# Performance work log

Measured on AMD Instinct MI355X. Metric: run time of the kernel, lower is better.

Reference implementation:

```python
import jax, jax.numpy as jnp
import numpy as np

VOCAB = 65
N_EMBD = 32
HEAD = 16
BLOCK = 8
B = 65536


def setup_inputs() -> dict:
    key = jax.random.key(0)
    ks = jax.random.split(key, 12)
    idx = jax.random.randint(ks[0], (B, BLOCK), 0, VOCAB)
    targets = jax.random.randint(ks[1], (B, BLOCK), 0, VOCAB)
    s = 0.02
    tok_emb = jax.random.normal(ks[2], (VOCAB, N_EMBD), jnp.float32) * s
    pos_emb = jax.random.normal(ks[3], (BLOCK, N_EMBD), jnp.float32) * s
    Wk = jax.random.normal(ks[4], (N_EMBD, HEAD), jnp.float32) * s
    bk = jnp.zeros((HEAD,), jnp.float32)
    Wq = jax.random.normal(ks[5], (N_EMBD, HEAD), jnp.float32) * s
    bq = jnp.zeros((HEAD,), jnp.float32)
    Wv = jax.random.normal(ks[6], (N_EMBD, HEAD), jnp.float32) * s
    bv = jnp.zeros((HEAD,), jnp.float32)
    Wlm = jax.random.normal(ks[7], (HEAD, VOCAB), jnp.float32) * s
    blm = jnp.zeros((VOCAB,), jnp.float32)
    return {"idx": idx, "targets": targets, "tok_emb": tok_emb, "pos_emb": pos_emb,
            "Wk": Wk, "bk": bk, "Wq": Wq, "bq": bq, "Wv": Wv, "bv": bv,
            "Wlm": Wlm, "blm": blm}


def reference(idx, targets, tok_emb, pos_emb, Wk, bk, Wq, bq, Wv, bv, Wlm, blm):
    Bsz, T = idx.shape
    x = tok_emb[idx] + pos_emb[None, :T, :]                  # (B,T,C)
    k = x @ Wk + bk                                          # (B,T,H)
    q = x @ Wq + bq
    wei = jnp.einsum('bth,bsh->bts', q, k) * (HEAD ** -0.5)  # (B,T,T)
    tril = jnp.tril(jnp.ones((T, T), bool))
    wei = jnp.where(tril[None], wei, -jnp.inf)
    # NOTE: original torch code uses F.softmax(wei, dim=1) — over the QUERY axis.
    wei = jax.nn.softmax(wei, axis=1)
    v = x @ Wv + bv
    attn = jnp.einsum('bts,bsh->bth', wei, v)                # (B,T,H)
    logits = attn @ Wlm + blm                                # (B,T,V)
    logits_flat = logits.reshape(Bsz * T, VOCAB)
    tgt_flat = targets.reshape(Bsz * T)
    logp = jax.nn.log_softmax(logits_flat, axis=-1)
    loss = -jnp.mean(jnp.take_along_axis(logp, tgt_flat[:, None], axis=-1))
    return logits_flat, loss
```

## Files before the change

### kernel.cpp

```cpp
#include <hip/hip_runtime.h>

#define NVOC 65
#define NE   32
#define HD   16
#define NB   65536
#define NROWS (NB * 8)
#define NLOG  (NROWS * NVOC)


static __device__ __forceinline__ float readlane_f(float v, int l) {
  return __uint_as_float(__builtin_amdgcn_readlane(__float_as_uint(v), l));
}

__global__ __launch_bounds__(1024) void bigram_tables(
    const float* __restrict__ tok, const float* __restrict__ pos,
    const float* __restrict__ Wk, const float* __restrict__ bk,
    const float* __restrict__ Wq, const float* __restrict__ bq,
    const float* __restrict__ Wv, const float* __restrict__ bv,
    const float* __restrict__ Wlm, float* __restrict__ ws)
{
  __shared__ float S[8416];
  const int tid = threadIdx.x;
  const int bid = blockIdx.x;
  for (int o = tid; o < 2080; o += 1024) S[o] = tok[o];
  for (int o = tid; o < 256;  o += 1024) S[2080 + o] = pos[o];
  for (int o = tid; o < 512;  o += 1024) {
    S[2336 + o] = Wq[o]; S[2848 + o] = Wk[o]; S[3360 + o] = Wv[o];
  }
  for (int o = tid; o < 1040; o += 1024) S[3872 + o] = Wlm[o];
  __syncthreads();

  for (int o = tid; o < 1168; o += 1024) {
    if (o < 1040) {
      const int a = o >> 4, h = o & 15;
      float sq = 0.f, sk = 0.f, sv = 0.f;
      #pragma unroll
      for (int c = 0; c < NE; ++c) {
        const float e = S[a*32 + c];
        sq = fmaf(e, S[2336 + c*16 + h], sq);
        sk = fmaf(e, S[2848 + c*16 + h], sk);
        sv = fmaf(e, S[3360 + c*16 + h], sv);
      }
      S[4912 + o] = sq; S[5952 + o] = sk; S[6992 + o] = sv;
    } else {
      const int o2 = o - 1040, t = o2 >> 4, h = o2 & 15;
      float sq = bq[h], sk = bk[h], sv = bv[h];
      #pragma unroll
      for (int c = 0; c < NE; ++c) {
        const float e = S[2080 + t*32 + c];
        sq = fmaf(e, S[2336 + c*16 + h], sq);
        sk = fmaf(e, S[2848 + c*16 + h], sk);
        sv = fmaf(e, S[3360 + c*16 + h], sv);
      }
      S[8032 + o2] = sq; S[8160 + o2] = sk; S[8288 + o2] = sv;
    }
  }
  __syncthreads();

  float* wsTab = ws + 16;
  const int lo = bid * 632;
  const int hi = (lo + 632 < 10074) ? lo + 632 : 10074;
  for (int o = lo + tid; o < hi; o += 1024) {
    float r = 0.f; int dst;
    if (o < 4225) {
      const int a = o / 65, b = o % 65;
      #pragma unroll
      for (int h = 0; h < HD; ++h) r = fmaf(S[4912 + a*16 + h], S[5952 + b*16 + h], r);
      r *= 0.25f; dst = o;
    } else if (o < 4745) {
      const int o2 = o - 4225, a = o2 >> 3, s2 = o2 & 7;
      #pragma unroll
      for (int h = 0; h < HD; ++h) r = fmaf(S[4912 + a*16 + h], S[8160 + s2*16 + h], r);
      r *= 0.25f; dst = 8450 + o2;
    } else if (o < 5265) {
      const int o2 = o - 4745, t2 = o2 / 65, b = o2 % 65;
      #pragma unroll
      for (int h = 0; h < HD; ++h) r = fmaf(S[8032 + t2*16 + h], S[5952 + b*16 + h], r);
      r *= 0.25f; dst = 8970 + o2;
    } else if (o < 5329) {
      const int o2 = o - 5265, t2 = o2 >> 3, s2 = o2 & 7;
      #pragma unroll
      for (int h = 0; h < HD; ++h) r = fmaf(S[8032 + t2*16 + h], S[8160 + s2*16 + h], r);
      r *= 0.25f; dst = 9490 + o2;
    } else if (o < 9554) {
      const int o2 = o - 5329, a = o2 / 65, j = o2 % 65;
      #pragma unroll
      for (int h = 0; h < HD; ++h) r = fmaf(S[6992 + a*16 + h], S[3872 + h*65 + j], r);
      dst = 4225 + o2;
    } else {
      const int o2 = o - 9554, s2 = o2 / 65, j = o2 % 65;
      #pragma unroll
      for (int h = 0; h < HD; ++h) r = fmaf(S[8288 + s2*16 + h], S[3872 + h*65 + j], r);
      dst = o;
    }
    wsTab[dst] = r;
  }
}

__global__ __launch_bounds__(512, 8) void bigram_main(
    const int* __restrict__ idx, const int* __restrict__ tgt,
    const float* __restrict__ blm, const float* __restrict__ ws,
    float* __restrict__ wsout, float* __restrict__ out)
{
  __shared__ __align__(16) float S[10074];
  __shared__ float red[8];
  const int tid = threadIdx.x;
  const int lane = tid & 63;
  const int w    = tid >> 6;
  const int t    = lane >> 3;
  const int s    = lane & 7;
  const int u    = lane & 7;
  const int gw = blockIdx.x * 8 + w;
  const int iv = idx[gw*64 + lane];
  const int tv = tgt[gw*64 + lane];
  const float blmj  = blm[lane];
  const float blm64 = blm[64];
  const float* wsTab = ws + 16;
  {
    const float4* t4 = (const float4*)wsTab;
    float4* s4 = (float4*)S;
    for (int o = tid; o < 2518; o += 512) s4[o] = t4[o];
    if (tid < 2) S[10072 + tid] = wsTab[10072 + tid];
  }
  __syncthreads();

  const int gwu = __builtin_amdgcn_readfirstlane(gw);
  float* __restrict__ outw = out + (size_t)gwu * 4160u;
  const unsigned l65p64 = (unsigned)lane * 65u + 64u;
  const bool lane8m = (lane < 8);

  const float g4 = S[9490 + lane];
  float pvl[8], pvl64[8];
  #pragma unroll
  for (int k = 0; k < 8; ++k) {
    pvl[k]   = S[9554 + k*65 + lane];
    pvl64[k] = S[9554 + k*65 + 64];
  }
  const bool b0 = (lane & 1) != 0, b1 = (lane & 2) != 0, b2 = (lane & 4) != 0;

  float wsm_cur;
  {
    const int av  = __shfl(iv, s);
    const int a_t = __shfl(iv, t);
    float wr = S[a_t*65 + av] + S[8450 + a_t*8 + s] + S[8970 + t*65 + av] + g4;
    float e = (t >= s) ? __expf(wr) : 0.f;
    float sm = e;
    sm += __shfl_xor(sm, 8); sm += __shfl_xor(sm, 16); sm += __shfl_xor(sm, 32);
    wsm_cur = __fdividef(e, sm);
  }

  float acc_lsm = 0.f, tl = 0.f;
  for (int itb = 0; itb < 8; ++itb) {
    const int base  = itb * 8;
    const int basen = ((itb + 1) & 7) * 8;
    float msr[8], Ms64[8];
    #pragma unroll
    for (int k = 0; k < 8; ++k) {
      const int ak = __builtin_amdgcn_readlane(iv, base + k);
      msr[k]  = S[4225 + ak*65 + lane];
      Ms64[k] = S[4225 + ak*65 + 64] + pvl64[k];
    }
    const int av_n  = __shfl(iv, basen + s);
    const int a_tn  = __shfl(iv, basen + t);
    float Ms[8];
    #pragma unroll
    for (int k = 0; k < 8; ++k) Ms[k] = msr[k] + pvl[k];
    const float wr_n = S[a_tn*65 + av_n] + S[8450 + a_tn*8 + s]
                     + S[8970 + t*65 + av_n] + g4;
    float e_n = (t >= s) ? __expf(wr_n) : 0.f;
    float lg64v = blm64;
    #pragma unroll
    for (int k = 0; k < 8; ++k) {
      const float wk_row = __shfl(wsm_cur, u*8 + k);
      lg64v = fmaf(wk_row, Ms64[k], lg64v);
    }
    float sm_n = e_n;
    sm_n += __shfl_xor(sm_n, 8);
    const unsigned vo = (unsigned)itb * 520u + (unsigned)lane;
    if (lane8m) outw[(unsigned)itb * 520u + l65p64] = lg64v;
    {
      const int tgu = __shfl(tv, base + u);
      tl += (lane8m && tgu == 64) ? lg64v : 0.f;
    }
    float ee[8];
    #pragma unroll
    for (int tt = 0; tt < 4; ++tt) {
      float lg = blmj;
      #pragma unroll
      for (int k = 0; k <= tt; ++k) {
        const float wk = readlane_f(wsm_cur, tt*8 + k);
        lg = fmaf(wk, Ms[k], lg);
      }
      outw[vo + tt*65] = lg;
      ee[tt] = __expf(lg);
      const int tg = __builtin_amdgcn_readlane(tv, base + tt);
      tl += (lane == tg) ? lg : 0.f;
    }
    sm_n += __shfl_xor(sm_n, 16);
    #pragma unroll
    for (int tt = 4; tt < 8; ++tt) {
      float lg = blmj;
      #pragma unroll
      for (int k = 0; k <= tt; ++k) {
        const float wk = readlane_f(wsm_cur, tt*8 + k);
        lg = fmaf(wk, Ms[k], lg);
      }
      outw[vo + tt*65] = lg;
      ee[tt] = __expf(lg);
      const int tg = __builtin_amdgcn_readlane(tv, base + tt);
      tl += (lane == tg) ? lg : 0.f;
    }
    sm_n += __shfl_xor(sm_n, 32);
    float k0 = b0 ? ee[1] : ee[0], s0 = b0 ? ee[0] : ee[1];
    float k1 = b0 ? ee[3] : ee[2], s1 = b0 ? ee[2] : ee[3];
    float k2 = b0 ? ee[5] : ee[4], s2 = b0 ? ee[4] : ee[5];
    float k3 = b0 ? ee[7] : ee[6], s3 = b0 ? ee[6] : ee[7];
    k0 += __shfl_xor(s0, 1); k1 += __shfl_xor(s1, 1);
    k2 += __shfl_xor(s2, 1); k3 += __shfl_xor(s3, 1);
    float m0 = b1 ? k1 : k0, t0 = b1 ? k0 : k1;
    float m1 = b1 ? k3 : k2, t1 = b1 ? k2 : k3;
    m0 += __shfl_xor(t0, 2); m1 += __shfl_xor(t1, 2);
    float r = b2 ? m1 : m0,  t2 = b2 ? m0 : m1;
    r += __shfl_xor(t2, 4);
    if (lane8m) r += __expf(lg64v);
    r += __shfl_xor(r, 8); r += __shfl_xor(r, 16); r += __shfl_xor(r, 32);
    acc_lsm += __log2f(r);
    wsm_cur = __fdividef(e_n, sm_n);
  }
  float v = acc_lsm * (0.6931471805599453f * 0.125f) - tl;
  v += __shfl_xor(v, 1); v += __shfl_xor(v, 2);  v += __shfl_xor(v, 4);
  v += __shfl_xor(v, 8); v += __shfl_xor(v, 16); v += __shfl_xor(v, 32);
  if (lane == 0) red[w] = v;
  __syncthreads();
  if (tid == 0) {
    wsout[10112 + blockIdx.x] = red[0] + red[1] + red[2] + red[3]
                              + red[4] + red[5] + red[6] + red[7];
  }
}

__global__ __launch_bounds__(1024) void bigram_fin2(
    const float* __restrict__ ws, float* __restrict__ out)
{
  __shared__ float r[16];
  const int tid = threadIdx.x;
  float v = ws[10112 + tid];
  v += __shfl_xor(v, 1); v += __shfl_xor(v, 2);  v += __shfl_xor(v, 4);
  v += __shfl_xor(v, 8); v += __shfl_xor(v, 16); v += __shfl_xor(v, 32);
  if ((tid & 63) == 0) r[tid >> 6] = v;
  __syncthreads();
  if (tid == 0) {
    float a = 0.f;
    #pragma unroll
    for (int i = 0; i < 16; ++i) a += r[i];
    out[NLOG] = a * (1.0f / (float)NROWS);
  }
}

extern "C" void kernel_launch(void* const* d_in, const int* in_sizes, int n_in,
                              void* d_out, int out_size, void* d_ws, size_t ws_size,
                              hipStream_t stream) {
  const int* idx = (const int*)d_in[0];
  const int* tgt = (const int*)d_in[1];
  float* ws = (float*)d_ws;
  float* out = (float*)d_out;

  bigram_tables<<<16, 1024, 0, stream>>>((const float*)d_in[2], (const float*)d_in[3],
                                         (const float*)d_in[4], (const float*)d_in[5],
                                         (const float*)d_in[6], (const float*)d_in[7],
                                         (const float*)d_in[8], (const float*)d_in[9],
                                         (const float*)d_in[10], ws);
  bigram_main<<<1024, 512, 0, stream>>>(idx, tgt, (const float*)d_in[11], ws, ws, out);
  bigram_fin2<<<1, 1024, 0, stream>>>(ws, out);
}
```

Before: 180.7 us.

## Use DPP/swizzle/permlane reductions and software-pipeline row softmax reduction

```diff
diff --git a/kernel.cpp b/kernel.cpp
--- a/kernel.cpp
+++ b/kernel.cpp
@@ -10,6 +10,29 @@
 
 static __device__ __forceinline__ float readlane_f(float v, int l) {
   return __uint_as_float(__builtin_amdgcn_readlane(__float_as_uint(v), l));
+}
+template<int C>
+static __device__ __forceinline__ float dppx(float x) {
+  return __int_as_float(__builtin_amdgcn_update_dpp(
+      __float_as_int(x), __float_as_int(x), C, 0xF, 0xF, true));
+}
+#define DPP_X1 0xB1
+#define DPP_X2 0x4E
+template<int P>
+static __device__ __forceinline__ float swz(float x) {
+  return __int_as_float(__builtin_amdgcn_ds_swizzle(__float_as_int(x), P));
+}
+#define SWZ_X4 0x101F
+#define SWZ_X8 0x201F
+static __device__ __forceinline__ float permsum16(float x) {
+  auto pr = __builtin_amdgcn_permlane16_swap(__float_as_uint(x),
+                                             __float_as_uint(x), false, false);
+  return __uint_as_float(pr[0]) + __uint_as_float(pr[1]);
+}
+static __device__ __forceinline__ float permsum32(float x) {
+  auto pr = __builtin_amdgcn_permlane32_swap(__float_as_uint(x),
+                                             __float_as_uint(x), false, false);
+  return __uint_as_float(pr[0]) + __uint_as_float(pr[1]);
 }
 
 __global__ __launch_bounds__(1024) void bigram_tables(
@@ -109,10 +132,12 @@
   const int w    = tid >> 6;
   const int t    = lane >> 3;
   const int s    = lane & 7;
-  const int u    = lane & 7;
   const int gw = blockIdx.x * 8 + w;
-  const int iv = idx[gw*64 + lane];
-  const int tv = tgt[gw*64 + lane];
+  const int gwu = __builtin_amdgcn_readfirstlane(gw);
+  const int* __restrict__ idxw = idx + (gwu << 6);
+  const int* __restrict__ tgtw = tgt + (gwu << 6);
+  const int iv = idxw[lane];
+  const int tv = tgtw[lane];
   const float blmj  = blm[lane];
   const float blm64 = blm[64];
   const float* wsTab = ws + 16;
@@ -124,109 +149,99 @@
   }
   __syncthreads();
 
-  const int gwu = __builtin_amdgcn_readfirstlane(gw);
   float* __restrict__ outw = out + (size_t)gwu * 4160u;
-  const unsigned l65p64 = (unsigned)lane * 65u + 64u;
-  const bool lane8m = (lane < 8);
+  const bool s8   = (s == 0);
+  const bool diag = (t == s);
+  const unsigned vo64 = (unsigned)t * 65u + 64u;
 
   const float g4 = S[9490 + lane];
-  float pvl[8], pvl64[8];
+  float pvl[8];
   #pragma unroll
-  for (int k = 0; k < 8; ++k) {
-    pvl[k]   = S[9554 + k*65 + lane];
-    pvl64[k] = S[9554 + k*65 + 64];
-  }
+  for (int k = 0; k < 8; ++k) pvl[k] = S[9554 + k*65 + lane];
+  const float pvl64s = S[9554 + s*65 + 64];
   const bool b0 = (lane & 1) != 0, b1 = (lane & 2) != 0, b2 = (lane & 4) != 0;
 
-  float wsm_cur;
-  {
-    const int av  = __shfl(iv, s);
-    const int a_t = __shfl(iv, t);
-    float wr = S[a_t*65 + av] + S[8450 + a_t*8 + s] + S[8970 + t*65 + av] + g4;
-    float e = (t >= s) ? __expf(wr) : 0.f;
-    float sm = e;
-    sm += __shfl_xor(sm, 8); sm += __shfl_xor(sm, 16); sm += __shfl_xor(sm, 32);
-    wsm_cur = __fdividef(e, sm);
-  }
-
   float acc_lsm = 0.f, tl = 0.f;
-  for (int itb = 0; itb < 8; ++itb) {
-    const int base  = itb * 8;
-    const int basen = ((itb + 1) & 7) * 8;
-    float msr[8], Ms64[8];
-    #pragma unroll
-    for (int k = 0; k < 8; ++k) {
-      const int ak = __builtin_amdgcn_readlane(iv, base + k);
-      msr[k]  = S[4225 + ak*65 + lane];
-      Ms64[k] = S[4225 + ak*65 + 64] + pvl64[k];
-    }
-    const int av_n  = __shfl(iv, basen + s);
-    const int a_tn  = __shfl(iv, basen + t);
-    float Ms[8];
-    #pragma unroll
-    for (int k = 0; k < 8; ++k) Ms[k] = msr[k] + pvl[k];
-    const float wr_n = S[a_tn*65 + av_n] + S[8450 + a_tn*8 + s]
-                     + S[8970 + t*65 + av_n] + g4;
-    float e_n = (t >= s) ? __expf(wr_n) : 0.f;
-    float lg64v = blm64;
-    #pragma unroll
-    for (int k = 0; k < 8; ++k) {
-      const float wk_row = __shfl(wsm_cur, u*8 + k);
-      lg64v = fmaf(wk_row, Ms64[k], lg64v);
-    }
-    float sm_n = e_n;
-    sm_n += __shfl_xor(sm_n, 8);
-    const unsigned vo = (unsigned)itb * 520u + (unsigned)lane;
-    if (lane8m) outw[(unsigned)itb * 520u + l65p64] = lg64v;
-    {
-      const int tgu = __shfl(tv, base + u);
-      tl += (lane8m && tgu == 64) ? lg64v : 0.f;
-    }
-    float ee[8];
-    #pragma unroll
-    for (int tt = 0; tt < 4; ++tt) {
-      float lg = blmj;
-      #pragma unroll
-      for (int k = 0; k <= tt; ++k) {
-        const float wk = readlane_f(wsm_cur, tt*8 + k);
-        lg = fmaf(wk, Ms[k], lg);
-      }
-      outw[vo + tt*65] = lg;
-      ee[tt] = __expf(lg);
-      const int tg = __builtin_amdgcn_readlane(tv, base + tt);
-      tl += (lane == tg) ? lg : 0.f;
-    }
-    sm_n += __shfl_xor(sm_n, 16);
-    #pragma unroll
-    for (int tt = 4; tt < 8; ++tt) {
-      float lg = blmj;
-      #pragma unroll
-      for (int k = 0; k <= tt; ++k) {
-        const float wk = readlane_f(wsm_cur, tt*8 + k);
-        lg = fmaf(wk, Ms[k], lg);
-      }
-      outw[vo + tt*65] = lg;
-      ee[tt] = __expf(lg);
-      const int tg = __builtin_amdgcn_readlane(tv, base + tt);
-      tl += (lane == tg) ? lg : 0.f;
-    }
-    sm_n += __shfl_xor(sm_n, 32);
+  float eeP[8];
+  float lg64P = 0.f;
+  auto reduce_row = [&](const float* ee, float lg64) {
     float k0 = b0 ? ee[1] : ee[0], s0 = b0 ? ee[0] : ee[1];
     float k1 = b0 ? ee[3] : ee[2], s1 = b0 ? ee[2] : ee[3];
     float k2 = b0 ? ee[5] : ee[4], s2 = b0 ? ee[4] : ee[5];
     float k3 = b0 ? ee[7] : ee[6], s3 = b0 ? ee[6] : ee[7];
-    k0 += __shfl_xor(s0, 1); k1 += __shfl_xor(s1, 1);
-    k2 += __shfl_xor(s2, 1); k3 += __shfl_xor(s3, 1);
+    k0 += dppx<DPP_X1>(s0); k1 += dppx<DPP_X1>(s1);
+    k2 += dppx<DPP_X1>(s2); k3 += dppx<DPP_X1>(s3);
     float m0 = b1 ? k1 : k0, t0 = b1 ? k0 : k1;
     float m1 = b1 ? k3 : k2, t1 = b1 ? k2 : k3;
-    m0 += __shfl_xor(t0, 2); m1 += __shfl_xor(t1, 2);
-    float r = b2 ? m1 : m0,  t2 = b2 ? m0 : m1;
-    r += __shfl_xor(t2, 4);
-    if (lane8m) r += __expf(lg64v);
-    r += __shfl_xor(r, 8); r += __shfl_xor(r, 16); r += __shfl_xor(r, 32);
+    m0 += dppx<DPP_X2>(t0); m1 += dppx<DPP_X2>(t1);
+    float r = b2 ? m1 : m0,  t2v = b2 ? m0 : m1;
+    r += swz<SWZ_X4>(t2v);
+    if (diag) r += __expf(lg64);
+    r += swz<SWZ_X8>(r);
+    r = permsum16(r); r = permsum32(r);
     acc_lsm += __log2f(r);
+  };
+
+  float wsm_cur; int av_cur;
+  {
+    const int av0 = idxw[s];
+    const int at0 = idxw[t];
+    const float wr = S[at0*65 + av0] + S[8450 + at0*8 + s]
+                   + S[8970 + t*65 + av0] + g4;
+    const float e = (t >= s) ? __expf(wr) : 0.f;
+    float sm = e + swz<SWZ_X8>(e);
+    sm = permsum16(sm); sm = permsum32(sm);
+    wsm_cur = __fdividef(e, sm);
+    av_cur = av0;
+  }
+
+  for (int itb = 0; itb < 8; ++itb) {
+    const int base  = itb * 8;
+    const int basen = ((itb + 1) & 7) * 8;
+    const int av_n = idxw[basen + s];
+    const int at_n = idxw[basen + t];
+    const int tg_c = tgtw[base + t];
+    float ms[8];
+    #pragma unroll
+    for (int k = 0; k < 8; ++k) {
+      const int ak = __builtin_amdgcn_readlane(iv, base + k);
+      ms[k] = S[4225 + ak*65 + lane];
+    }
+    const float m64 = S[4225 + av_cur*65 + 64] + pvl64s;
+    if (itb > 0) reduce_row(eeP, lg64P);
+    const float wr_n = S[at_n*65 + av_n] + S[8450 + at_n*8 + s]
+                     + S[8970 + t*65 + av_n] + g4;
+    const float e_n = (t >= s) ? __expf(wr_n) : 0.f;
+    float c64 = wsm_cur * m64;
+    c64 += dppx<DPP_X1>(c64);
+    c64 += dppx<DPP_X2>(c64);
+    c64 += swz<SWZ_X4>(c64);
+    const float lg64v = c64 + blm64;
+    if (s8) outw[(unsigned)(base*65) + vo64] = lg64v;
+    tl += (s8 && tg_c == 64) ? lg64v : 0.f;
+    float sm_n = e_n + swz<SWZ_X8>(e_n);
+    #pragma unroll
+    for (int k = 0; k < 8; ++k) ms[k] += pvl[k];
+    const unsigned vo = (unsigned)(base*65) + (unsigned)lane;
+    #pragma unroll
+    for (int tt = 0; tt < 8; ++tt) {
+      float lg = blmj;
+      #pragma unroll
+      for (int k = 0; k <= tt; ++k) {
+        const float wk = readlane_f(wsm_cur, tt*8 + k);
+        lg = fmaf(wk, ms[k], lg);
+      }
+      outw[vo + tt*65] = lg;
+      eeP[tt] = __expf(lg);
+      const int tg = __builtin_amdgcn_readlane(tv, base + tt);
+      tl += (lane == tg) ? lg : 0.f;
+    }
+    sm_n = permsum16(sm_n); sm_n = permsum32(sm_n);
     wsm_cur = __fdividef(e_n, sm_n);
-  }
+    av_cur  = av_n;
+    lg64P   = lg64v;
+  }
+  reduce_row(eeP, lg64P);
   float v = acc_lsm * (0.6931471805599453f * 0.125f) - tl;
   v += __shfl_xor(v, 1); v += __shfl_xor(v, 2);  v += __shfl_xor(v, 4);
   v += __shfl_xor(v, 8); v += __shfl_xor(v, 16); v += __shfl_xor(v, 32);
```

After: 180.7 us. No clear change (-0.0%).
